# Performance work log

Hardware: AMD Instinct MI355X
Metric: run time of the kernel (lower is better)

The kernel has to match this reference:

```python
import jax, jax.numpy as jnp
import numpy as np

B, N, PL = 8, 961, 50          # batch, sequence_len=(64-4)//2+1 squared, patch_len=3*4^2+2
HID = 200                       # int(4.0 * patch_len)
D, H, HD = 768, 12, 64          # embed_dim, num_heads, head_dim
MP = 1536                       # int(2.0 * embed_dim)


def setup_inputs() -> dict:
    key = jax.random.key(0)
    ks = jax.random.split(key, 16)
    w = lambda k, i, o: jax.random.normal(k, (i, o), jnp.float32) / np.float32(np.sqrt(i))
    b = lambda k, o: jax.random.normal(k, (o,), jnp.float32) * np.float32(0.01)
    return {
        "x": jax.random.normal(ks[0], (B, N, PL), jnp.float32),
        "W1": w(ks[1], PL, HID),   "b1": b(ks[2], HID),
        "W2": w(ks[3], HID, HID),  "b2": b(ks[4], HID),
        "W3": w(ks[5], HID, HID),  "b3": b(ks[6], HID),
        "W4": w(ks[7], HID, D),    "b4": b(ks[8], D),
        "Wruv": w(ks[9], D, 3 * D), "bruv": b(ks[10], 3 * D),
        "Wp1": w(ks[11], N * HD, MP), "bp1": b(ks[12], MP),
        "Wp2": w(ks[13], MP, 1),      "bp2": b(ks[14], 1),
    }


def reference(x, W1, b1, W2, b2, W3, b3, W4, b4, Wruv, bruv, Wp1, bp1, Wp2, bp2):
    Bs, Ns, _ = x.shape
    # pointwise MLP (note: original has NO activations, just stacked Linears)
    h = x.reshape(Bs * Ns, -1)
    h = (((h @ W1 + b1) @ W2 + b2) @ W3 + b3) @ W4 + b4           # (B*N, D)
    # fused r,u,v projection -> (3, H, B, N, HD)
    ruv = (h @ Wruv + bruv).reshape(Bs, Ns, 3, H, HD).transpose(2, 3, 0, 1, 4)
    r, u, v = ruv[0], ruv[1], ruv[2]                               # each (H, B, N, HD)
    attn = jax.nn.softmax(jnp.einsum('hbnd,hbmd->hbnm', r, u), axis=-1)
    o = jnp.einsum('hbnm,hbmd->hbnd', attn, v).reshape(H, Bs, Ns * HD)
    # per-head projection: weights are SHARED across heads (list built via [m]*H)
    q = (jnp.einsum('hbm,mp->hbp', o, Wp1) + bp1) @ Wp2 + bp2      # (H, B, 1)
    return q[..., 0].T                                             # (B, 12)
```

## Files before the change

### kernel.cpp

```cpp
#include <hip/hip_runtime.h>
#include <hip/hip_bf16.h>

#define TPB 256

typedef __attribute__((ext_vector_type(8))) short bf16x8;
typedef __attribute__((ext_vector_type(4))) float f32x4;

static __device__ __forceinline__ unsigned short f2bf(float f) {
  union { float f; unsigned int u; } x; x.f = f;
  unsigned int r = x.u + 0x7FFF + ((x.u >> 16) & 1);
  return (unsigned short)(r >> 16);
}
static __device__ __forceinline__ float bf2f(unsigned short h) {
  union { unsigned int u; float f; } x; x.u = ((unsigned int)h) << 16;
  return x.f;
}

#define MFMA16(a, b, c) __builtin_amdgcn_mfma_f32_16x16x32_bf16(a, b, c, 0, 0, 0)

__global__ __launch_bounds__(TPB) void fold_wp_fused_k(
    const float* __restrict__ A, const float* __restrict__ lastrow,
    const float* __restrict__ W, const float* __restrict__ bias,
    float* __restrict__ C, int K, int Nc, int gemmBlocks,
    const float* __restrict__ Wp1, const float* __restrict__ Wp2,
    float* __restrict__ wfold, int wpStart, int wpCount,
    const float* __restrict__ bp1, const float* __restrict__ bp2,
    float* __restrict__ out)
{
  __shared__ float As[64][68];
  __shared__ float Ws[64][68];
  __shared__ float red[4];
  int bid = blockIdx.x, tid = threadIdx.x;

  if (bid >= gemmBlocks) {
    int u = bid - gemmBlocks;
    int wv = tid >> 6, lane = tid & 63;
    if (u >= wpCount) {
      float s = 0.f;
      for (int i = tid; i < 1536; i += TPB) s += bp1[i] * Wp2[i];
#pragma unroll
      for (int off = 32; off >= 1; off >>= 1) s += __shfl_xor(s, off, 64);
      if (lane == 0) red[wv] = s;
      __syncthreads();
      if (tid < 96) out[tid] = red[0] + red[1] + red[2] + red[3] + bp2[0];
      return;
    }
    float* w2 = &As[0][0];
    for (int i = tid; i < 1536; i += TPB) w2[i] = Wp2[i];
    __syncthreads();
    int m = (wpStart + u) * 4 + wv;
    const float* row = Wp1 + (size_t)m * 1536;
    float s = 0.f;
#pragma unroll
    for (int k = 0; k < 6; ++k) {
      float4 a  = *(const float4*)(row + k * 256 + lane * 4);
      float4 ww = *(const float4*)&w2[k * 256 + lane * 4];
      s += a.x * ww.x + a.y * ww.y + a.z * ww.z + a.w * ww.w;
    }
#pragma unroll
    for (int off = 32; off >= 1; off >>= 1) s += __shfl_xor(s, off, 64);
    if (lane == 0) wfold[m] = s;
    return;
  }

  int col0 = bid * 64;
  int ty = tid >> 4, tx = tid & 15;
  float acc[4][4] = {};
  for (int k0 = 0; k0 < K; k0 += 64) {
#pragma unroll
    for (int i = 0; i < 16; ++i) {
      int idx = tid + i * TPB;
      int r = idx >> 6, kk = idx & 63;
      int gk = k0 + kk;
      float v = 0.f;
      if (gk < K) {
        if (r < 50) v = A[(size_t)r * K + gk];
        else if (r == 50) v = lastrow[gk];
      }
      As[kk][r] = v;
    }
#pragma unroll
    for (int i = 0; i < 16; ++i) {
      int idx = tid + i * TPB;
      int kk = idx >> 6, cc = idx & 63;
      int gk = k0 + kk, gc = col0 + cc;
      float v = 0.f;
      if (gk < K && gc < Nc) v = W[(size_t)gk * Nc + gc];
      Ws[kk][cc] = v;
    }
    __syncthreads();
#pragma unroll 8
    for (int kk = 0; kk < 64; ++kk) {
      float4 a4 = *(const float4*)&As[kk][ty * 4];
      float4 b4 = *(const float4*)&Ws[kk][tx * 4];
      float av[4] = {a4.x, a4.y, a4.z, a4.w};
      float bv[4] = {b4.x, b4.y, b4.z, b4.w};
#pragma unroll
      for (int i = 0; i < 4; ++i)
#pragma unroll
        for (int j = 0; j < 4; ++j)
          acc[i][j] = fmaf(av[i], bv[j], acc[i][j]);
    }
    __syncthreads();
  }
#pragma unroll
  for (int i = 0; i < 4; ++i) {
    int gr = ty * 4 + i;
    if (gr >= 51) continue;
#pragma unroll
    for (int j = 0; j < 4; ++j) {
      int gc = col0 + tx * 4 + j;
      if (gc >= Nc) continue;
      float v = acc[i][j];
      if (gr == 50) v += bias[gc];
      C[(size_t)gr * Nc + gc] = v;
    }
  }
}

__global__ __launch_bounds__(TPB) void fold4_fused_k(
    const float* __restrict__ aug3,
    const float* __restrict__ Wruv,
    const float* __restrict__ bruv,
    unsigned short* __restrict__ WfTh, unsigned short* __restrict__ WfTl,
    float* __restrict__ bfv,
    const float* __restrict__ x,
    unsigned short* __restrict__ xh, unsigned short* __restrict__ xl,
    unsigned short* __restrict__ xT,
    const float* __restrict__ Wp1, const float* __restrict__ Wp2,
    float* __restrict__ wfold, int wpStart, int wpCount)
{
  __shared__ float As[64][68];
  __shared__ float Ws[64][68];
  int bid = blockIdx.x, tid = threadIdx.x;

  if (bid >= 157) {
    int u = bid - 157;
    if (u >= wpCount) return;
    int wv = tid >> 6, lane = tid & 63;
    float* w2 = &As[0][0];
    for (int i = tid; i < 1536; i += TPB) w2[i] = Wp2[i];
    __syncthreads();
    int m = (wpStart + u) * 4 + wv;
    const float* row = Wp1 + (size_t)m * 1536;
    float s = 0.f;
#pragma unroll
    for (int k = 0; k < 6; ++k) {
      float4 a  = *(const float4*)(row + k * 256 + lane * 4);
      float4 ww = *(const float4*)&w2[k * 256 + lane * 4];
      s += a.x * ww.x + a.y * ww.y + a.z * ww.z + a.w * ww.w;
    }
#pragma unroll
    for (int off = 32; off >= 1; off >>= 1) s += __shfl_xor(s, off, 64);
    if (lane == 0) wfold[m] = s;
    return;
  }

  if (bid >= 36) {
    int row0 = (bid - 36) * 64;
#pragma unroll
    for (int i = 0; i < 16; ++i) {
      int idx = tid + i * TPB;
      int row = row0 + (idx >> 6), cc = idx & 63;
      if (row >= 7688) continue;
      float v = 0.f;
      if (cc < 50) v = x[(size_t)row * 50 + cc];
      else if (cc == 50) v = 1.0f;
      unsigned short hi = f2bf(v);
      xh[(size_t)row * 64 + cc] = hi;
      xl[(size_t)row * 64 + cc] = f2bf(v - bf2f(hi));
      int bb = row / 961;
      int nl = row - bb * 961;
      xT[((size_t)bb * 64 + cc) * 968 + nl] = hi;
    }
    return;
  }

  const int K = 768, Nc = 2304;
  const float* lastrow = aug3 + (size_t)50 * 768;
  int col0 = bid * 64;
  int ty = tid >> 4, tx = tid & 15;
  float acc[4][4] = {};
  for (int k0 = 0; k0 < K; k0 += 64) {
#pragma unroll
    for (int i = 0; i < 16; ++i) {
      int idx = tid + i * TPB;
      int r = idx >> 6, kk = idx & 63;
      int gk = k0 + kk;
      float v = 0.f;
      if (r < 50) v = aug3[(size_t)r * K + gk];
      else if (r == 50) v = lastrow[gk];
      As[kk][r] = v;
    }
#pragma unroll
    for (int i = 0; i < 16; ++i) {
      int idx = tid + i * TPB;
      int kk = idx >> 6, cc = idx & 63;
      Ws[kk][cc] = Wruv[(size_t)(k0 + kk) * Nc + col0 + cc];
    }
    __syncthreads();
#pragma unroll 8
    for (int kk = 0; kk < 64; ++kk) {
      float4 a4 = *(const float4*)&As[kk][ty * 4];
      float4 b4 = *(const float4*)&Ws[kk][tx * 4];
      float av[4] = {a4.x, a4.y, a4.z, a4.w};
      float bv[4] = {b4.x, b4.y, b4.z, b4.w};
#pragma unroll
      for (int i = 0; i < 4; ++i)
#pragma unroll
        for (int j = 0; j < 4; ++j)
          acc[i][j] = fmaf(av[i], bv[j], acc[i][j]);
    }
    __syncthreads();
  }
#pragma unroll
  for (int i = 0; i < 4; ++i) {
    int gr = ty * 4 + i;
    if (gr >= 51) continue;
#pragma unroll
    for (int j = 0; j < 4; ++j) {
      int gc = col0 + tx * 4 + j;
      float v = acc[i][j];
      if (gr == 50) {
        bfv[gc] = v + bruv[gc];
      } else {
        unsigned short hi = f2bf(v);
        size_t el = (size_t)gc * 64 + gr;
        WfTh[el] = hi;
        WfTl[el] = f2bf(v - bf2f(hi));
      }
    }
  }
}

__global__ __launch_bounds__(TPB) void prep_k(
    const unsigned short* __restrict__ WfTh,
    const unsigned short* __restrict__ WfTl,
    const float* __restrict__ bfv,
    const float* __restrict__ wfold,
    unsigned short* __restrict__ Mth,
    unsigned short* __restrict__ Mtl,
    float* __restrict__ wvf)
{
  __shared__ float Al[64][64];
  __shared__ float Bl[64][64];
  int bid = blockIdx.x, tid = threadIdx.x;

  if (bid < 12) {
    int h = bid;
    for (int idx = tid; idx < 4096; idx += TPB) {
      int d = idx >> 6, i = idx & 63;
      int colr = h * 64 + d, colu = 768 + h * 64 + d;
      float wr = 0.f, wu = 0.f;
      if (i < 50) {
        wr = bf2f(WfTh[(size_t)colr * 64 + i]) + bf2f(WfTl[(size_t)colr * 64 + i]);
        wu = bf2f(WfTh[(size_t)colu * 64 + i]) + bf2f(WfTl[(size_t)colu * 64 + i]);
      } else if (i == 50) {
        wr = bfv[colr];
        wu = bfv[colu];
      }
      Al[d][i] = wr;
      Bl[d][i] = wu;
    }
    __syncthreads();
    for (int idx = tid; idx < 4096; idx += TPB) {
      int j = idx >> 6, i = idx & 63;
      float m = 0.f;
#pragma unroll 8
      for (int d = 0; d < 64; ++d) m += Al[d][i] * Bl[d][j];
      unsigned short hi = f2bf(m);
      size_t el = ((size_t)h * 64 + j) * 64 + i;
      Mth[el] = hi;
      Mtl[el] = f2bf(m - bf2f(hi));
    }
    return;
  }

  int u = bid - 12;
  int h = u >> 4, nb = u & 15;
  for (int idx = tid; idx < 4096; idx += TPB) {
    int d = idx >> 6, f = idx & 63;
    int colv = 1536 + h * 64 + d;
    float wv = 0.f;
    if (f < 50)
      wv = bf2f(WfTh[(size_t)colv * 64 + f]) + bf2f(WfTl[(size_t)colv * 64 + f]);
    else if (f == 50)
      wv = bfv[colv];
    Al[d][f] = wv;
    int nl = idx >> 6, dd = idx & 63;
    int n = nb * 64 + nl;
    Bl[nl][dd] = (n <= 960) ? wfold[(size_t)n * 64 + dd] : 0.f;
  }
  __syncthreads();
  for (int idx = tid; idx < 4096; idx += TPB) {
    int nl = idx >> 6, f = idx & 63;
    int n = nb * 64 + nl;
    if (n > 960) continue;
    float s = 0.f;
#pragma unroll 8
    for (int d = 0; d < 64; ++d) s += Bl[nl][d] * Al[d][f];
    wvf[((size_t)h * 961 + n) * 64 + f] = s;
  }
}

__global__ __launch_bounds__(512) void attn_x_k(
    const unsigned short* __restrict__ xh,
    const unsigned short* __restrict__ xl,
    const unsigned short* __restrict__ xT,
    const unsigned short* __restrict__ Mth,
    const unsigned short* __restrict__ Mtl,
    const float* __restrict__ wvf,
    float* __restrict__ out)
{
  __shared__ unsigned short sh[24576];
  int bid = blockIdx.x;
  int tid = threadIdx.x;

  int qb = bid & 7, hb = bid >> 3;
  int h = hb >> 3, b = hb & 7;
  int n0 = qb * 128;
  int w = tid >> 6, lane = tid & 63;
  int g = lane >> 4, c = lane & 15;
  int xb = b * 961;
  unsigned short* Kbuf[2] = {sh, sh + 4096};
  unsigned short* Vbuf[2] = {sh + 8192, sh + 12288};
  unsigned short* pw = sh + 16384 + w * 1024;

  int srow = tid >> 3, ss = tid & 7;
  int sel = srow * 64 + 8 * (ss ^ (srow & 7));
  const unsigned short* ksrc = xh + (size_t)xb * 64 + ss * 8;
  const unsigned short* vsrc = xT + ((size_t)b * 64 + srow) * 968 + ss * 8;
  int4 kv0 = *(const int4*)(ksrc + (size_t)srow * 64);
  int4 vv0 = *(const int4*)(vsrc);

  int qrow = n0 + w * 16 + c;
  if (qrow > 960) qrow = 960;
  size_t rowb = (size_t)(xb + qrow) * 64;
  bf16x8 axh0 = *(const bf16x8*)&xh[rowb + g * 8];
  bf16x8 axh1 = *(const bf16x8*)&xh[rowb + 32 + g * 8];
  bf16x8 axl0 = *(const bf16x8*)&xl[rowb + g * 8];
  bf16x8 axl1 = *(const bf16x8*)&xl[rowb + 32 + g * 8];

  f32x4 zero4 = {0.f, 0.f, 0.f, 0.f};
  f32x4 zacc[4] = {zero4, zero4, zero4, zero4};
#pragma unroll
  for (int ct = 0; ct < 4; ++ct) {
    int j = c * 4 + ct;
    size_t mb = ((size_t)h * 64 + j) * 64;
    bf16x8 bh0 = *(const bf16x8*)&Mth[mb + g * 8];
    bf16x8 bh1 = *(const bf16x8*)&Mth[mb + 32 + g * 8];
    bf16x8 bl0 = *(const bf16x8*)&Mtl[mb + g * 8];
    bf16x8 bl1 = *(const bf16x8*)&Mtl[mb + 32 + g * 8];
    zacc[ct] = MFMA16(axh0, bh0, zacc[ct]);
    zacc[ct] = MFMA16(axh1, bh1, zacc[ct]);
    zacc[ct] = MFMA16(axl0, bh0, zacc[ct]);
    zacc[ct] = MFMA16(axl1, bh1, zacc[ct]);
    zacc[ct] = MFMA16(axh0, bl0, zacc[ct]);
    zacc[ct] = MFMA16(axh1, bl1, zacc[ct]);
  }
#pragma unroll
  for (int r = 0; r < 4; ++r) {
    unsigned short pb[4];
#pragma unroll
    for (int ct = 0; ct < 4; ++ct) pb[ct] = f2bf(zacc[ct][r]);
    int q = g * 4 + r;
    int e0 = (c * 4) ^ ((q & 7) * 8);
    *(unsigned int*)&pw[q * 64 + e0] =
        (unsigned int)pb[0] | ((unsigned int)pb[1] << 16);
    *(unsigned int*)&pw[q * 64 + e0 + 2] =
        (unsigned int)pb[2] | ((unsigned int)pb[3] << 16);
  }
  bf16x8 zf0 = *(const bf16x8*)&pw[c * 64 + ((g * 8) ^ ((c & 7) * 8))];
  bf16x8 zf1 = *(const bf16x8*)&pw[c * 64 + ((32 + g * 8) ^ ((c & 7) * 8))];

  bf16x8 ones;
#pragma unroll
  for (int i = 0; i < 8; ++i) ones[i] = (short)0x3F80;

  *(int4*)&Kbuf[0][sel] = kv0;
  *(int4*)&Vbuf[0][sel] = vv0;
  __syncthreads();

  f32x4 pxacc[4] = {zero4, zero4, zero4, zero4};
  f32x4 rowacc = zero4;

  unsigned short* Kc = Kbuf[0];
  unsigned short* Vc = Vbuf[0];
  unsigned short* Kn = Kbuf[1];
  unsigned short* Vn = Vbuf[1];

  for (int kt = 0; kt < 16; ++kt) {
    int4 pk, pv;
    bool pre = (kt < 15);
    if (pre) {
      int keyg = (kt + 1) * 64 + srow;
      int kcl = keyg > 960 ? 960 : keyg;
      pk = *(const int4*)(ksrc + (size_t)kcl * 64);
      pv = *(const int4*)(vsrc + (kt + 1) * 64);
    }

    f32x4 sa[4] = {zero4, zero4, zero4, zero4};
    __builtin_amdgcn_s_setprio(1);
#pragma unroll
    for (int ct = 0; ct < 4; ++ct) {
      int key = c * 4 + ct;
      int sw = (key & 7) * 8;
      bf16x8 k0 = *(const bf16x8*)&Kc[key * 64 + ((g * 8) ^ sw)];
      bf16x8 k1 = *(const bf16x8*)&Kc[key * 64 + ((32 + g * 8) ^ sw)];
      sa[ct] = MFMA16(zf0, k0, sa[ct]);
      sa[ct] = MFMA16(zf1, k1, sa[ct]);
    }
    __builtin_amdgcn_s_setprio(0);

    if (kt < 15) {
#pragma unroll
      for (int r = 0; r < 4; ++r) {
        unsigned short pb[4];
#pragma unroll
        for (int ct = 0; ct < 4; ++ct)
          pb[ct] = f2bf(__expf(sa[ct][r]));
        int q = g * 4 + r;
        int e0 = (c * 4) ^ ((q & 7) * 8);
        *(unsigned int*)&pw[q * 64 + e0] =
            (unsigned int)pb[0] | ((unsigned int)pb[1] << 16);
        *(unsigned int*)&pw[q * 64 + e0 + 2] =
            (unsigned int)pb[2] | ((unsigned int)pb[3] << 16);
      }
    } else {
#pragma unroll
      for (int r = 0; r < 4; ++r) {
        unsigned short pb[4];
#pragma unroll
        for (int ct = 0; ct < 4; ++ct) {
          int keyg = kt * 64 + c * 4 + ct;
          pb[ct] = (keyg <= 960) ? f2bf(__expf(sa[ct][r])) : (unsigned short)0;
        }
        int q = g * 4 + r;
        int e0 = (c * 4) ^ ((q & 7) * 8);
        *(unsigned int*)&pw[q * 64 + e0] =
            (unsigned int)pb[0] | ((unsigned int)pb[1] << 16);
        *(unsigned int*)&pw[q * 64 + e0 + 2] =
            (unsigned int)pb[2] | ((unsigned int)pb[3] << 16);
      }
    }

    if (pre) {
      *(int4*)&Kn[sel] = pk;
      *(int4*)&Vn[sel] = pv;
    }

    __builtin_amdgcn_s_setprio(1);
#pragma unroll
    for (int kk = 0; kk < 2; ++kk) {
      bf16x8 pa = *(const bf16x8*)&pw[c * 64 + ((kk * 32 + g * 8) ^ ((c & 7) * 8))];
      rowacc = MFMA16(pa, ones, rowacc);
#pragma unroll
      for (int dt = 0; dt < 4; ++dt) {
        int d = dt * 16 + c;
        bf16x8 vf = *(const bf16x8*)&Vc[d * 64 + ((kk * 32 + g * 8) ^ ((d & 7) * 8))];
        pxacc[dt] = MFMA16(pa, vf, pxacc[dt]);
      }
    }
    __builtin_amdgcn_s_setprio(0);

    __syncthreads();
    unsigned short* t;
    t = Kc; Kc = Kn; Kn = t;
    t = Vc; Vc = Vn; Vn = t;
  }

  int nbase = n0 + w * 16 + g * 4;
  float part = 0.f;
#pragma unroll
  for (int r = 0; r < 4; ++r) {
    int n = nbase + r;
    if (n > 960) continue;
    float inv = 1.f / rowacc[r];
    const float* wv = wvf + ((size_t)h * 961 + n) * 64;
#pragma unroll
    for (int dt = 0; dt < 4; ++dt)
      part += pxacc[dt][r] * inv * wv[dt * 16 + c];
  }
#pragma unroll
  for (int off = 32; off >= 1; off >>= 1) part += __shfl_xor(part, off, 64);
  float* red = (float*)sh;
  if (lane == 0) red[w] = part;
  __syncthreads();
  if (tid == 0) {
    float tot = red[0] + red[1] + red[2] + red[3] +
                red[4] + red[5] + red[6] + red[7];
    atomicAdd(&out[b * 12 + h], tot);
  }
}

extern "C" void kernel_launch(void* const* d_in, const int* in_sizes, int n_in,
                              void* d_out, int out_size, void* d_ws, size_t ws_size,
                              hipStream_t stream)
{
  const float* x    = (const float*)d_in[0];
  const float* W1   = (const float*)d_in[1];
  const float* b1   = (const float*)d_in[2];
  const float* W2   = (const float*)d_in[3];
  const float* b2   = (const float*)d_in[4];
  const float* W3   = (const float*)d_in[5];
  const float* b3   = (const float*)d_in[6];
  const float* W4   = (const float*)d_in[7];
  const float* b4   = (const float*)d_in[8];
  const float* Wruv = (const float*)d_in[9];
  const float* bruv = (const float*)d_in[10];
  const float* Wp1  = (const float*)d_in[11];
  const float* bp1  = (const float*)d_in[12];
  const float* Wp2  = (const float*)d_in[13];
  const float* bp2  = (const float*)d_in[14];
  float* out = (float*)d_out;

  char* base = (char*)d_ws;
  size_t off = 0;
  auto alloc = [&](size_t bytes) -> void* {
    void* p = base + off;
    off = (off + bytes + 255) & ~(size_t)255;
    return p;
  };
  float* aug1  = (float*)alloc(51 * 200 * 4);
  float* aug2  = (float*)alloc(51 * 200 * 4);
  float* aug3  = (float*)alloc(51 * 768 * 4);
  unsigned short* WfTh = (unsigned short*)alloc((size_t)2304 * 64 * 2);
  unsigned short* WfTl = (unsigned short*)alloc((size_t)2304 * 64 * 2);
  unsigned short* xh   = (unsigned short*)alloc((size_t)(7688 + 64) * 64 * 2);
  unsigned short* xl   = (unsigned short*)alloc((size_t)(7688 + 64) * 64 * 2);
  unsigned short* xT   = (unsigned short*)alloc((size_t)8 * 64 * 968 * 2 + 1024);
  unsigned short* Mth  = (unsigned short*)alloc((size_t)12 * 64 * 64 * 2);
  unsigned short* Mtl  = (unsigned short*)alloc((size_t)12 * 64 * 64 * 2);
  float* wvf   = (float*)alloc((size_t)12 * 961 * 64 * 4);
  float* bfv   = (float*)alloc(2304 * 4);
  float* wfold = (float*)alloc(61504 * 4);
  if (off > ws_size) return;

  dim3 tb(TPB);

  fold_wp_fused_k<<<dim3(4 + 3000 + 1), tb, 0, stream>>>(
      W1, b1, W2, b2, aug1, 200, 200, 4,
      Wp1, Wp2, wfold, 0, 3000, bp1, bp2, out);
  fold_wp_fused_k<<<dim3(4 + 3000), tb, 0, stream>>>(
      aug1, aug1 + 50 * 200, W3, b3, aug2, 200, 200, 4,
      Wp1, Wp2, wfold, 3000, 3000, bp1, bp2, out);
  fold_wp_fused_k<<<dim3(12 + 3000), tb, 0, stream>>>(
      aug2, aug2 + 50 * 200, W4, b4, aug3, 200, 768, 12,
      Wp1, Wp2, wfold, 6000, 3000, bp1, bp2, out);

  fold4_fused_k<<<dim3(157 + 6376), tb, 0, stream>>>(
      aug3, Wruv, bruv, WfTh, WfTl, bfv, x, xh, xl, xT,
      Wp1, Wp2, wfold, 9000, 6376);

  prep_k<<<dim3(204), tb, 0, stream>>>(WfTh, WfTl, bfv, wfold, Mth, Mtl, wvf);

  attn_x_k<<<dim3(768), dim3(512), 0, stream>>>(xh, xl, xT, Mth, Mtl, wvf, out);
}
```

Baseline: 318.6 us.

## Fold weight chain as a tree and compute per-head RUV products inside prep kernel

Reassociates the chain of stacked linear weight folds into a two-level tree (W1·W2 and W3·W4 in parallel, then combined), cutting the serial launch chain from five kernels to three. The full Wruv fold into a bf16 hi/lo intermediate is dropped; each prep block instead computes its own head's projection of the folded weights directly from Wruv in fp32. The log2(e) scale is folded into the score matrix so the attention kernel can use exp2f instead of __expf. The trade-off is redundant per-block Wruv reads and scalar LDS GEMMs in the prep kernel, which may lengthen that stage.

```diff
diff --git a/kernel.cpp b/kernel.cpp
--- a/kernel.cpp
+++ b/kernel.cpp
@@ -18,52 +18,12 @@
 
 #define MFMA16(a, b, c) __builtin_amdgcn_mfma_f32_16x16x32_bf16(a, b, c, 0, 0, 0)
 
-__global__ __launch_bounds__(TPB) void fold_wp_fused_k(
+static __device__ __forceinline__ void aug_gemm_tile(
     const float* __restrict__ A, const float* __restrict__ lastrow,
     const float* __restrict__ W, const float* __restrict__ bias,
-    float* __restrict__ C, int K, int Nc, int gemmBlocks,
-    const float* __restrict__ Wp1, const float* __restrict__ Wp2,
-    float* __restrict__ wfold, int wpStart, int wpCount,
-    const float* __restrict__ bp1, const float* __restrict__ bp2,
-    float* __restrict__ out)
-{
-  __shared__ float As[64][68];
-  __shared__ float Ws[64][68];
-  __shared__ float red[4];
-  int bid = blockIdx.x, tid = threadIdx.x;
-
-  if (bid >= gemmBlocks) {
-    int u = bid - gemmBlocks;
-    int wv = tid >> 6, lane = tid & 63;
-    if (u >= wpCount) {
-      float s = 0.f;
-      for (int i = tid; i < 1536; i += TPB) s += bp1[i] * Wp2[i];
-#pragma unroll
-      for (int off = 32; off >= 1; off >>= 1) s += __shfl_xor(s, off, 64);
-      if (lane == 0) red[wv] = s;
-      __syncthreads();
-      if (tid < 96) out[tid] = red[0] + red[1] + red[2] + red[3] + bp2[0];
-      return;
-    }
-    float* w2 = &As[0][0];
-    for (int i = tid; i < 1536; i += TPB) w2[i] = Wp2[i];
-    __syncthreads();
-    int m = (wpStart + u) * 4 + wv;
-    const float* row = Wp1 + (size_t)m * 1536;
-    float s = 0.f;
-#pragma unroll
-    for (int k = 0; k < 6; ++k) {
-      float4 a  = *(const float4*)(row + k * 256 + lane * 4);
-      float4 ww = *(const float4*)&w2[k * 256 + lane * 4];
-      s += a.x * ww.x + a.y * ww.y + a.z * ww.z + a.w * ww.w;
-    }
-#pragma unroll
-    for (int off = 32; off >= 1; off >>= 1) s += __shfl_xor(s, off, 64);
-    if (lane == 0) wfold[m] = s;
-    return;
-  }
-
-  int col0 = bid * 64;
+    float* __restrict__ C, int K, int Nc, int MR, int row0, int col0,
+    int tid, float (*As)[68], float (*Ws)[68])
+{
   int ty = tid >> 4, tx = tid & 15;
   float acc[4][4] = {};
   for (int k0 = 0; k0 < K; k0 += 64) {
@@ -71,11 +31,11 @@
     for (int i = 0; i < 16; ++i) {
       int idx = tid + i * TPB;
       int r = idx >> 6, kk = idx & 63;
-      int gk = k0 + kk;
+      int gk = k0 + kk, grow = row0 + r;
       float v = 0.f;
       if (gk < K) {
-        if (r < 50) v = A[(size_t)r * K + gk];
-        else if (r == 50) v = lastrow[gk];
+        if (grow < MR) v = A[(size_t)grow * K + gk];
+        else if (grow == MR) v = lastrow[gk];
       }
       As[kk][r] = v;
     }
@@ -105,59 +65,71 @@
   }
 #pragma unroll
   for (int i = 0; i < 4; ++i) {
-    int gr = ty * 4 + i;
-    if (gr >= 51) continue;
+    int grow = row0 + ty * 4 + i;
+    if (grow > MR) continue;
 #pragma unroll
     for (int j = 0; j < 4; ++j) {
       int gc = col0 + tx * 4 + j;
       if (gc >= Nc) continue;
       float v = acc[i][j];
-      if (gr == 50) v += bias[gc];
-      C[(size_t)gr * Nc + gc] = v;
-    }
-  }
-}
-
-__global__ __launch_bounds__(TPB) void fold4_fused_k(
-    const float* __restrict__ aug3,
-    const float* __restrict__ Wruv,
-    const float* __restrict__ bruv,
-    unsigned short* __restrict__ WfTh, unsigned short* __restrict__ WfTl,
-    float* __restrict__ bfv,
+      if (grow == MR) v += bias[gc];
+      C[(size_t)grow * Nc + gc] = v;
+    }
+  }
+}
+
+static __device__ __forceinline__ void wp_unit(
+    const float* __restrict__ Wp1, const float* __restrict__ Wp2,
+    float* __restrict__ wfold, int unit, int tid, float* w2lds)
+{
+  int wv = tid >> 6, lane = tid & 63;
+  for (int i = tid; i < 1536; i += TPB) w2lds[i] = Wp2[i];
+  __syncthreads();
+  int m = unit * 4 + wv;
+  const float* row = Wp1 + (size_t)m * 1536;
+  float s = 0.f;
+#pragma unroll
+  for (int k = 0; k < 6; ++k) {
+    float4 a  = *(const float4*)(row + k * 256 + lane * 4);
+    float4 ww = *(const float4*)&w2lds[k * 256 + lane * 4];
+    s += a.x * ww.x + a.y * ww.y + a.z * ww.z + a.w * ww.w;
+  }
+#pragma unroll
+  for (int off = 32; off >= 1; off >>= 1) s += __shfl_xor(s, off, 64);
+  if (lane == 0) wfold[m] = s;
+}
+
+__global__ __launch_bounds__(TPB) void tree1_k(
+    const float* __restrict__ W1, const float* __restrict__ b1,
+    const float* __restrict__ W2, const float* __restrict__ b2,
+    const float* __restrict__ W3, const float* __restrict__ b3,
+    const float* __restrict__ W4, const float* __restrict__ b4,
+    float* __restrict__ aug12, float* __restrict__ aug34,
     const float* __restrict__ x,
     unsigned short* __restrict__ xh, unsigned short* __restrict__ xl,
     unsigned short* __restrict__ xT,
     const float* __restrict__ Wp1, const float* __restrict__ Wp2,
-    float* __restrict__ wfold, int wpStart, int wpCount)
+    float* __restrict__ wfold,
+    const float* __restrict__ bp1, const float* __restrict__ bp2,
+    float* __restrict__ out)
 {
   __shared__ float As[64][68];
   __shared__ float Ws[64][68];
+  __shared__ float red[4];
   int bid = blockIdx.x, tid = threadIdx.x;
 
-  if (bid >= 157) {
-    int u = bid - 157;
-    if (u >= wpCount) return;
-    int wv = tid >> 6, lane = tid & 63;
-    float* w2 = &As[0][0];
-    for (int i = tid; i < 1536; i += TPB) w2[i] = Wp2[i];
-    __syncthreads();
-    int m = (wpStart + u) * 4 + wv;
-    const float* row = Wp1 + (size_t)m * 1536;
-    float s = 0.f;
-#pragma unroll
-    for (int k = 0; k < 6; ++k) {
-      float4 a  = *(const float4*)(row + k * 256 + lane * 4);
-      float4 ww = *(const float4*)&w2[k * 256 + lane * 4];
-      s += a.x * ww.x + a.y * ww.y + a.z * ww.z + a.w * ww.w;
-    }
-#pragma unroll
-    for (int off = 32; off >= 1; off >>= 1) s += __shfl_xor(s, off, 64);
-    if (lane == 0) wfold[m] = s;
+  if (bid < 4) {
+    aug_gemm_tile(W1, b1, W2, b2, aug12, 200, 200, 50, 0, bid * 64, tid, As, Ws);
     return;
   }
-
-  if (bid >= 36) {
-    int row0 = (bid - 36) * 64;
+  if (bid < 52) {
+    int u = bid - 4;
+    aug_gemm_tile(W3, b3, W4, b4, aug34, 200, 768, 200,
+                  (u / 12) * 64, (u % 12) * 64, tid, As, Ws);
+    return;
+  }
+  if (bid < 173) {
+    int row0 = (bid - 52) * 64;
 #pragma unroll
     for (int i = 0; i < 16; ++i) {
       int idx = tid + i * TPB;
@@ -175,99 +147,92 @@
     }
     return;
   }
-
-  const int K = 768, Nc = 2304;
-  const float* lastrow = aug3 + (size_t)50 * 768;
-  int col0 = bid * 64;
-  int ty = tid >> 4, tx = tid & 15;
-  float acc[4][4] = {};
-  for (int k0 = 0; k0 < K; k0 += 64) {
-#pragma unroll
-    for (int i = 0; i < 16; ++i) {
-      int idx = tid + i * TPB;
-      int r = idx >> 6, kk = idx & 63;
-      int gk = k0 + kk;
-      float v = 0.f;
-      if (r < 50) v = aug3[(size_t)r * K + gk];
-      else if (r == 50) v = lastrow[gk];
-      As[kk][r] = v;
-    }
-#pragma unroll
-    for (int i = 0; i < 16; ++i) {
-      int idx = tid + i * TPB;
-      int kk = idx >> 6, cc = idx & 63;
-      Ws[kk][cc] = Wruv[(size_t)(k0 + kk) * Nc + col0 + cc];
-    }
-    __syncthreads();
-#pragma unroll 8
-    for (int kk = 0; kk < 64; ++kk) {
-      float4 a4 = *(const float4*)&As[kk][ty * 4];
-      float4 b4 = *(const float4*)&Ws[kk][tx * 4];
-      float av[4] = {a4.x, a4.y, a4.z, a4.w};
-      float bv[4] = {b4.x, b4.y, b4.z, b4.w};
-#pragma unroll
-      for (int i = 0; i < 4; ++i)
-#pragma unroll
-        for (int j = 0; j < 4; ++j)
-          acc[i][j] = fmaf(av[i], bv[j], acc[i][j]);
-    }
-    __syncthreads();
-  }
-#pragma unroll
-  for (int i = 0; i < 4; ++i) {
-    int gr = ty * 4 + i;
-    if (gr >= 51) continue;
-#pragma unroll
-    for (int j = 0; j < 4; ++j) {
-      int gc = col0 + tx * 4 + j;
-      float v = acc[i][j];
-      if (gr == 50) {
-        bfv[gc] = v + bruv[gc];
-      } else {
-        unsigned short hi = f2bf(v);
-        size_t el = (size_t)gc * 64 + gr;
-        WfTh[el] = hi;
-        WfTl[el] = f2bf(v - bf2f(hi));
-      }
-    }
-  }
-}
-
-__global__ __launch_bounds__(TPB) void prep_k(
-    const unsigned short* __restrict__ WfTh,
-    const unsigned short* __restrict__ WfTl,
-    const float* __restrict__ bfv,
+  if (bid < 7861) {
+    wp_unit(Wp1, Wp2, wfold, bid - 173, tid, &As[0][0]);
+    return;
+  }
+  {
+    int wv = tid >> 6, lane = tid & 63;
+    float s = 0.f;
+    for (int i = tid; i < 1536; i += TPB) s += bp1[i] * Wp2[i];
+#pragma unroll
+    for (int off = 32; off >= 1; off >>= 1) s += __shfl_xor(s, off, 64);
+    if (lane == 0) red[wv] = s;
+    __syncthreads();
+    if (tid < 96) out[tid] = red[0] + red[1] + red[2] + red[3] + bp2[0];
+  }
+}
+
+__global__ __launch_bounds__(TPB) void tree2_k(
+    const float* __restrict__ aug12, const float* __restrict__ aug34,
+    float* __restrict__ aug14,
+    const float* __restrict__ Wp1, const float* __restrict__ Wp2,
+    float* __restrict__ wfold)
+{
+  __shared__ float As[64][68];
+  __shared__ float Ws[64][68];
+  int bid = blockIdx.x, tid = threadIdx.x;
+  if (bid < 12) {
+    aug_gemm_tile(aug12, aug12 + (size_t)50 * 200, aug34,
+                  aug34 + (size_t)200 * 768, aug14,
+                  200, 768, 50, 0, bid * 64, tid, As, Ws);
+    return;
+  }
+  wp_unit(Wp1, Wp2, wfold, 7688 + (bid - 12), tid, &As[0][0]);
+}
+
+__global__ __launch_bounds__(TPB) void prep2_k(
+    const float* __restrict__ aug14,
+    const float* __restrict__ Wruv,
+    const float* __restrict__ bruv,
     const float* __restrict__ wfold,
     unsigned short* __restrict__ Mth,
     unsigned short* __restrict__ Mtl,
     float* __restrict__ wvf)
 {
-  __shared__ float Al[64][64];
-  __shared__ float Bl[64][64];
+  __shared__ float shm[14824];
   int bid = blockIdx.x, tid = threadIdx.x;
 
   if (bid < 12) {
     int h = bid;
-    for (int idx = tid; idx < 4096; idx += TPB) {
-      int d = idx >> 6, i = idx & 63;
-      int colr = h * 64 + d, colu = 768 + h * 64 + d;
-      float wr = 0.f, wu = 0.f;
-      if (i < 50) {
-        wr = bf2f(WfTh[(size_t)colr * 64 + i]) + bf2f(WfTl[(size_t)colr * 64 + i]);
-        wu = bf2f(WfTh[(size_t)colu * 64 + i]) + bf2f(WfTl[(size_t)colu * 64 + i]);
-      } else if (i == 50) {
-        wr = bfv[colr];
-        wu = bfv[colu];
-      }
-      Al[d][i] = wr;
-      Bl[d][i] = wu;
+    float* Ts = shm;
+    float* Wt = shm + 6630;
+    for (int t = tid; t < 6630; t += TPB) Ts[t] = 0.f;
+    __syncthreads();
+    for (int k0 = 0; k0 < 768; k0 += 64) {
+      for (int idx = tid; idx < 4096; idx += TPB) {
+        int kk = idx >> 6, d = idx & 63;
+        Wt[idx]        = Wruv[(size_t)(k0 + kk) * 2304 + h * 64 + d];
+        Wt[4096 + idx] = Wruv[(size_t)(k0 + kk) * 2304 + 768 + h * 64 + d];
+      }
+      __syncthreads();
+      for (int t = tid; t < 6528; t += TPB) {
+        int which = t >= 3264;
+        int e = t - which * 3264;
+        int i = e >> 6, d = e & 63;
+        float s = Ts[which * 3315 + i * 65 + d];
+        const float* ar = aug14 + (size_t)i * 768 + k0;
+        const float* wt = Wt + which * 4096 + d;
+#pragma unroll 16
+        for (int kk = 0; kk < 64; ++kk) s = fmaf(ar[kk], wt[kk * 64], s);
+        Ts[which * 3315 + i * 65 + d] = s;
+      }
+      __syncthreads();
+    }
+    if (tid < 128) {
+      int which = tid >> 6, d = tid & 63;
+      Ts[which * 3315 + 50 * 65 + d] += bruv[(which ? 768 : 0) + h * 64 + d];
     }
     __syncthreads();
     for (int idx = tid; idx < 4096; idx += TPB) {
       int j = idx >> 6, i = idx & 63;
       float m = 0.f;
-#pragma unroll 8
-      for (int d = 0; d < 64; ++d) m += Al[d][i] * Bl[d][j];
+      if (i < 51 && j < 51) {
+#pragma unroll 16
+        for (int d = 0; d < 64; ++d)
+          m = fmaf(Ts[i * 65 + d], Ts[3315 + j * 65 + d], m);
+        m *= 1.44269504088896f;
+      }
       unsigned short hi = f2bf(m);
       size_t el = ((size_t)h * 64 + j) * 64 + i;
       Mth[el] = hi;
@@ -278,18 +243,33 @@
 
   int u = bid - 12;
   int h = u >> 4, nb = u & 15;
+  float* Tv = shm;
+  float* Wt = shm + 3315;
+  float* Bw = shm + 7411;
+  for (int t = tid; t < 3315; t += TPB) Tv[t] = 0.f;
+  __syncthreads();
+  for (int k0 = 0; k0 < 768; k0 += 64) {
+    for (int idx = tid; idx < 4096; idx += TPB) {
+      int kk = idx >> 6, d = idx & 63;
+      Wt[idx] = Wruv[(size_t)(k0 + kk) * 2304 + 1536 + h * 64 + d];
+    }
+    __syncthreads();
+    for (int t = tid; t < 3264; t += TPB) {
+      int i = t >> 6, d = t & 63;
+      float s = Tv[i * 65 + d];
+      const float* ar = aug14 + (size_t)i * 768 + k0;
+      const float* wt = Wt + d;
+#pragma unroll 16
+      for (int kk = 0; kk < 64; ++kk) s = fmaf(ar[kk], wt[kk * 64], s);
+      Tv[i * 65 + d] = s;
+    }
+    __syncthreads();
+  }
+  if (tid < 64) Tv[50 * 65 + tid] += bruv[1536 + h * 64 + tid];
   for (int idx = tid; idx < 4096; idx += TPB) {
-    int d = idx >> 6, f = idx & 63;
-    int colv = 1536 + h * 64 + d;
-    float wv = 0.f;
-    if (f < 50)
-      wv = bf2f(WfTh[(size_t)colv * 64 + f]) + bf2f(WfTl[(size_t)colv * 64 + f]);
-    else if (f == 50)
-      wv = bfv[colv];
-    Al[d][f] = wv;
     int nl = idx >> 6, dd = idx & 63;
     int n = nb * 64 + nl;
-    Bl[nl][dd] = (n <= 960) ? wfold[(size_t)n * 64 + dd] : 0.f;
+    Bw[nl * 65 + dd] = (n <= 960) ? wfold[(size_t)n * 64 + dd] : 0.f;
   }
   __syncthreads();
   for (int idx = tid; idx < 4096; idx += TPB) {
@@ -297,8 +277,11 @@
     int n = nb * 64 + nl;
     if (n > 960) continue;
     float s = 0.f;
-#pragma unroll 8
-    for (int d = 0; d < 64; ++d) s += Bl[nl][d] * Al[d][f];
+    if (f < 51) {
+#pragma unroll 16
+      for (int d = 0; d < 64; ++d)
+        s = fmaf(Bw[nl * 65 + d], Tv[f * 65 + d], s);
+    }
     wvf[((size_t)h * 961 + n) * 64 + f] = s;
   }
 }
@@ -418,7 +401,7 @@
         unsigned short pb[4];
 #pragma unroll
         for (int ct = 0; ct < 4; ++ct)
-          pb[ct] = f2bf(__expf(sa[ct][r]));
+          pb[ct] = f2bf(exp2f(sa[ct][r]));
         int q = g * 4 + r;
         int e0 = (c * 4) ^ ((q & 7) * 8);
         *(unsigned int*)&pw[q * 64 + e0] =
@@ -433,7 +416,7 @@
 #pragma unroll
         for (int ct = 0; ct < 4; ++ct) {
           int keyg = kt * 64 + c * 4 + ct;
-          pb[ct] = (keyg <= 960) ? f2bf(__expf(sa[ct][r])) : (unsigned short)0;
+          pb[ct] = (keyg <= 960) ? f2bf(exp2f(sa[ct][r])) : (unsigned short)0;
         }
         int q = g * 4 + r;
         int e0 = (c * 4) ^ ((q & 7) * 8);
@@ -521,38 +504,27 @@
     off = (off + bytes + 255) & ~(size_t)255;
     return p;
   };
-  float* aug1  = (float*)alloc(51 * 200 * 4);
-  float* aug2  = (float*)alloc(51 * 200 * 4);
-  float* aug3  = (float*)alloc(51 * 768 * 4);
-  unsigned short* WfTh = (unsigned short*)alloc((size_t)2304 * 64 * 2);
-  unsigned short* WfTl = (unsigned short*)alloc((size_t)2304 * 64 * 2);
-  unsigned short* xh   = (unsigned short*)alloc((size_t)(7688 + 64) * 64 * 2);
-  unsigned short* xl   = (unsigned short*)alloc((size_t)(7688 + 64) * 64 * 2);
-  unsigned short* xT   = (unsigned short*)alloc((size_t)8 * 64 * 968 * 2 + 1024);
-  unsigned short* Mth  = (unsigned short*)alloc((size_t)12 * 64 * 64 * 2);
-  unsigned short* Mtl  = (unsigned short*)alloc((size_t)12 * 64 * 64 * 2);
+  float* aug12 = (float*)alloc((size_t)51 * 200 * 4);
+  float* aug34 = (float*)alloc((size_t)201 * 768 * 4);
+  float* aug14 = (float*)alloc((size_t)51 * 768 * 4);
+  unsigned short* xh  = (unsigned short*)alloc((size_t)(7688 + 64) * 64 * 2);
+  unsigned short* xl  = (unsigned short*)alloc((size_t)(7688 + 64) * 64 * 2);
+  unsigned short* xT  = (unsigned short*)alloc((size_t)8 * 64 * 968 * 2 + 1024);
+  unsigned short* Mth = (unsigned short*)alloc((size_t)12 * 64 * 64 * 2);
+  unsigned short* Mtl = (unsigned short*)alloc((size_t)12 * 64 * 64 * 2);
   float* wvf   = (float*)alloc((size_t)12 * 961 * 64 * 4);
-  float* bfv   = (float*)alloc(2304 * 4);
   float* wfold = (float*)alloc(61504 * 4);
   if (off > ws_size) return;
 
   dim3 tb(TPB);
 
-  fold_wp_fused_k<<<dim3(4 + 3000 + 1), tb, 0, stream>>>(
-      W1, b1, W2, b2, aug1, 200, 200, 4,
-      Wp1, Wp2, wfold, 0, 3000, bp1, bp2, out);
-  fold_wp_fused_k<<<dim3(4 + 3000), tb, 0, stream>>>(
-      aug1, aug1 + 50 * 200, W3, b3, aug2, 200, 200, 4,
-      Wp1, Wp2, wfold, 3000, 3000, bp1, bp2, out);
-  fold_wp_fused_k<<<dim3(12 + 3000), tb, 0, stream>>>(
-      aug2, aug2 + 50 * 200, W4, b4, aug3, 200, 768, 12,
-      Wp1, Wp2, wfold, 6000, 3000, bp1, bp2, out);
-
-  fold4_fused_k<<<dim3(157 + 6376), tb, 0, stream>>>(
-      aug3, Wruv, bruv, WfTh, WfTl, bfv, x, xh, xl, xT,
-      Wp1, Wp2, wfold, 9000, 6376);
-
-  prep_k<<<dim3(204), tb, 0, stream>>>(WfTh, WfTl, bfv, wfold, Mth, Mtl, wvf);
+  tree1_k<<<dim3(7862), tb, 0, stream>>>(
+      W1, b1, W2, b2, W3, b3, W4, b4, aug12, aug34,
+      x, xh, xl, xT, Wp1, Wp2, wfold, bp1, bp2, out);
+
+  tree2_k<<<dim3(7700), tb, 0, stream>>>(aug12, aug34, aug14, Wp1, Wp2, wfold);
+
+  prep2_k<<<dim3(204), tb, 0, stream>>>(aug14, Wruv, bruv, wfold, Mth, Mtl, wvf);
 
   attn_x_k<<<dim3(768), dim3(512), 0, stream>>>(xh, xl, xT, Mth, Mtl, wvf, out);
 }
```

After: 346.1 us. +8.6%, slower.
